# Kernel tuning notes

Measured on AMD Instinct MI355X. Metric: run time of the kernel, lower is better.

Reference implementation:

```python
import jax, jax.numpy as jnp
import numpy as np

N_ATOMS = 20000
N_EDGES = 640000
F = 128          # natom_basis
N_RADIAL = 20
CUTOFF = 5.0


def setup_inputs() -> dict:
    key = jax.random.key(0)
    ks = jax.random.split(key, 10)
    inp = {
        "q": jax.random.normal(ks[0], (N_ATOMS, F), dtype=jnp.float32),
        "mu": jax.random.normal(ks[1], (N_ATOMS, 3, F), dtype=jnp.float32),
        "edge_index": jax.random.randint(ks[2], (2, N_EDGES), 0, N_ATOMS, dtype=jnp.int32),
        "edge_weight": jax.random.normal(ks[3], (N_EDGES, 3), dtype=jnp.float32),
        # interaction_context_network: Linear(F,F) -> SiLU -> Linear(F,3F)
        "W1": jax.random.normal(ks[4], (F, F), dtype=jnp.float32) / np.sqrt(F),
        "b1": jnp.zeros((F,), dtype=jnp.float32),
        "W2": jax.random.normal(ks[5], (F, 3 * F), dtype=jnp.float32) / np.sqrt(F),
        "b2": jnp.zeros((3 * F,), dtype=jnp.float32),
        # filter_network: Linear(n_radial, 3F)
        "Wf": jax.random.normal(ks[6], (N_RADIAL, 3 * F), dtype=jnp.float32) / np.sqrt(N_RADIAL),
        "bf": jnp.zeros((3 * F,), dtype=jnp.float32),
    }
    return inp


def _sinc_radial(d):
    # Bessel/sinc basis: sin(n*pi*d/cutoff)/d, n = 1..n_radial
    n = jnp.arange(1, N_RADIAL + 1, dtype=jnp.float32)  # [R]
    return jnp.sin(d[:, None] * (n * np.pi / CUTOFF)) / d[:, None]  # [E,R]


def _cosine_envelope(d):
    env = 0.5 * (jnp.cos(d * (np.pi / CUTOFF)) + 1.0)
    return jnp.where(d < CUTOFF, env, 0.0)


def reference(q, mu, edge_index, edge_weight, W1, b1, W2, b2, Wf, bf):
    F_ = q.shape[-1]
    # dense per-node context MLP: [N, 3F]
    h = jax.nn.silu(q @ W1 + b1)
    x = h @ W2 + b2

    d = jnp.linalg.norm(edge_weight, axis=-1)              # [E]
    directions = edge_weight / d[:, None]                  # [E,3]
    basis = _sinc_radial(d)                                # [E,R]
    env = _cutoff = _cosine_envelope(d)[:, None]           # [E,1]
    filter_Wij = (basis @ Wf + bf) * env                   # [E,3F]

    idx_i = edge_index[0]
    idx_j = edge_index[1]
    xj = x[idx_j]                                          # [E,3F]
    muj = mu[idx_j]                                        # [E,3,F]

    xe = filter_Wij * xj
    dq, dmuR, dmumu = jnp.split(xe, 3, axis=-1)            # each [E,F]

    q_update = jax.ops.segment_sum(dq, idx_i, num_segments=q.shape[0])

    dmu = dmuR[:, None, :] * directions[:, :, None] + dmumu[:, None, :] * muj  # [E,3,F]
    mu_update = jax.ops.segment_sum(dmu, idx_i, num_segments=mu.shape[0])

    return (q + q_update, mu + mu_update)
```

## Files before the change

### kernel.cpp

```cpp
#include <hip/hip_runtime.h>
#include <hip/hip_bf16.h>

typedef unsigned int uint;
typedef unsigned short ushort;
typedef float v2f __attribute__((ext_vector_type(2)));

#define NATOMS 20000
#define NEDGES 640000
#define FD 128
#define F3 384
#define NR 20
#define MAPB 16
#define GAPB 2

__device__ __forceinline__ uint f2bfu(float f) {
  const uint u = __float_as_uint(f);
  return (u + 0x7FFFu + ((u >> 16) & 1u)) >> 16;
}
__device__ __forceinline__ float bflo(uint u) { return __uint_as_float(u << 16); }
__device__ __forceinline__ float bfhi(uint u) { return __uint_as_float(u & 0xFFFF0000u); }

__global__ __launch_bounds__(256) void hist_kernel(const int* __restrict__ eidx,
                                                   int* __restrict__ cnt) {
  const int e = blockIdx.x * 256 + threadIdx.x;
  if (e < NEDGES) atomicAdd(&cnt[eidx[e]], 1);
}

__global__ __launch_bounds__(512) void scan_kernel(const int* __restrict__ cnt,
                                                   int* __restrict__ off,
                                                   int* __restrict__ cursor) {
  __shared__ int part[512];
  const int t = threadIdx.x;
  const int CH = (NATOMS + 511) / 512;
  const int base = t * CH;
  int s = 0;
  for (int k = 0; k < CH; ++k) {
    const int idx = base + k;
    if (idx < NATOMS) s += cnt[idx];
  }
  part[t] = s;
  __syncthreads();
  if (t == 0) {
    int run = 0;
    for (int i = 0; i < 512; ++i) { const int tmp = part[i]; part[i] = run; run += tmp; }
    off[NATOMS] = run;
  }
  __syncthreads();
  int run = part[t];
  for (int k = 0; k < CH; ++k) {
    const int idx = base + k;
    if (idx < NATOMS) { off[idx] = run; cursor[idx] = run; run += cnt[idx]; }
  }
}

__global__ __launch_bounds__(256) void prep_kernel(
    const int* __restrict__ eidx, const float* __restrict__ ew,
    int* __restrict__ cursor, uint4* __restrict__ basisS)
{
  const int e = blockIdx.x * 256 + threadIdx.x;
  if (e >= NEDGES) return;
  const int i = eidx[e];
  const int j = eidx[NEDGES + e];
  const int pos = atomicAdd(&cursor[i], 1);

  const float w0 = ew[(size_t)e * 3 + 0];
  const float w1 = ew[(size_t)e * 3 + 1];
  const float w2 = ew[(size_t)e * 3 + 2];
  const float d = sqrtf(w0 * w0 + w1 * w1 + w2 * w2);
  const float invd = 1.f / d;
  float s1, c1;
  __sincosf(d * 0.628318530717958f, &s1, &c1);
  const float env = (d < 5.f) ? 0.5f * (c1 + 1.f) : 0.f;

  uint4 r0, r1;
  r0.x = __float_as_uint(s1 * env * invd);
  r0.y = __float_as_uint(2.f * c1);
  r0.z = __float_as_uint(env);
  r0.w = __float_as_uint(w0 * invd);
  r1.x = __float_as_uint(w1 * invd);
  r1.y = __float_as_uint(w2 * invd);
  r1.z = (uint)j;
  r1.w = 0u;
  basisS[(size_t)pos * 2 + 0] = r0;
  basisS[(size_t)pos * 2 + 1] = r1;
}

__global__ __launch_bounds__(128) void mlp_kernel(
    const float* __restrict__ q, const float* __restrict__ mu,
    const float* __restrict__ W1, const float* __restrict__ b1,
    const float* __restrict__ W2, const float* __restrict__ b2v,
    uint* __restrict__ xmp)
{
  __shared__ float qL[MAPB][FD];
  __shared__ float hL[MAPB][FD];
  const int t = threadIdx.x;
  const int a0 = blockIdx.x * MAPB;

  #pragma unroll
  for (int a = 0; a < MAPB; ++a) qL[a][t] = q[(size_t)(a0 + a) * FD + t];
  __syncthreads();

  float hacc[MAPB];
  const float bb1 = b1[t];
  #pragma unroll
  for (int a = 0; a < MAPB; ++a) hacc[a] = bb1;
  for (int i = 0; i < FD; ++i) {
    const float w = W1[(size_t)i * FD + t];
    #pragma unroll
    for (int a = 0; a < MAPB; ++a) hacc[a] += qL[a][i] * w;
  }
  #pragma unroll
  for (int a = 0; a < MAPB; ++a) hL[a][t] = hacc[a] / (1.f + __expf(-hacc[a]));
  __syncthreads();

  float x0[MAPB], x1[MAPB], x2[MAPB];
  const float c0 = b2v[t], c1 = b2v[FD + t], c2 = b2v[2 * FD + t];
  #pragma unroll
  for (int a = 0; a < MAPB; ++a) { x0[a] = c0; x1[a] = c1; x2[a] = c2; }
  for (int i = 0; i < FD; ++i) {
    const float w0 = W2[(size_t)i * F3 + t];
    const float w1 = W2[(size_t)i * F3 + FD + t];
    const float w2 = W2[(size_t)i * F3 + 2 * FD + t];
    #pragma unroll
    for (int a = 0; a < MAPB; ++a) {
      const float hv = hL[a][i];
      x0[a] += hv * w0; x1[a] += hv * w1; x2[a] += hv * w2;
    }
  }
  #pragma unroll
  for (int a = 0; a < MAPB; ++a) {
    const int n = a0 + a;
    const float* ma = mu + (size_t)n * F3;
    const float m0 = ma[t], m1 = ma[FD + t], m2 = ma[2 * FD + t];
    uint* dst = xmp + ((size_t)n * FD + t) * 3;
    dst[0] = f2bfu(x0[a]) | (f2bfu(x1[a]) << 16);
    dst[1] = f2bfu(x2[a]) | (f2bfu(m0) << 16);
    dst[2] = f2bfu(m1)    | (f2bfu(m2) << 16);
  }
}

__global__ __launch_bounds__(128, 3) void gather_kernel(
    const float* __restrict__ q, const float* __restrict__ mu,
    const uint* __restrict__ xmp,
    const float* __restrict__ Wf, const float* __restrict__ bfv,
    const int* __restrict__ off, const uint* __restrict__ basisS,
    float* __restrict__ out)
{
  __shared__ uint stage[64 * 8];
  __shared__ float fb[64][28];
  const int t = threadIdx.x;
  const int a0 = blockIdx.x * GAPB;

  v2f wf0[10], wf1[10], wf2[10];
  #pragma unroll
  for (int r = 0; r < 10; ++r) {
    wf0[r] = (v2f){Wf[(size_t)(2 * r) * F3 + t],       Wf[(size_t)(2 * r + 1) * F3 + t]};
    wf1[r] = (v2f){Wf[(size_t)(2 * r) * F3 + 128 + t], Wf[(size_t)(2 * r + 1) * F3 + 128 + t]};
    wf2[r] = (v2f){Wf[(size_t)(2 * r) * F3 + 256 + t], Wf[(size_t)(2 * r + 1) * F3 + 256 + t]};
  }
  const float bias0 = bfv[t], bias1 = bfv[128 + t], bias2 = bfv[256 + t];

  int a = a0;
  const int beg  = off[a0];
  const int pEnd = off[a0 + GAPB];
  int nxt = off[a + 1];
  float acq = 0.f, ac0 = 0.f, ac1 = 0.f, ac2 = 0.f;
  const size_t NQ = (size_t)NATOMS * FD;

  for (int cb = beg; cb < pEnd; cb += 64) {
    const int nn = min(64, pEnd - cb);
    __syncthreads();
    if (t < nn * 2) ((uint4*)stage)[t] = ((const uint4*)basisS)[(size_t)cb * 2 + t];
    __syncthreads();
    if (t < nn) {
      const uint4 r0 = ((const uint4*)stage)[t * 2];
      const uint4 r1 = ((const uint4*)stage)[t * 2 + 1];
      fb[t][20] = __uint_as_float(r0.z);
      fb[t][21] = __uint_as_float(r0.w);
      fb[t][22] = __uint_as_float(r1.x);
      fb[t][23] = __uint_as_float(r1.y);
      fb[t][24] = __uint_as_float(r1.z);
      float vp = 0.f, vc = __uint_as_float(r0.x);
      const float tc = __uint_as_float(r0.y);
      #pragma unroll
      for (int r = 0; r < NR; ++r) { fb[t][r] = vc; const float vn = tc * vc - vp; vp = vc; vc = vn; }
    }
    __syncthreads();

    uint pX, pY, pZ;
    {
      const uint j0 = __float_as_uint(fb[0][24]);
      const uint* xp = xmp + ((size_t)j0 * FD + t) * 3;
      pX = xp[0]; pY = xp[1]; pZ = xp[2];
    }

    for (int k = 0; k < nn; ++k) {
      const int g = cb + k;
      while (g == nxt) {
        out[(size_t)a * FD + t] = q[(size_t)a * FD + t] + acq;
        const size_t mi = (size_t)a * F3;
        out[NQ + mi + t]       = mu[mi + t]       + ac0;
        out[NQ + mi + 128 + t] = mu[mi + 128 + t] + ac1;
        out[NQ + mi + 256 + t] = mu[mi + 256 + t] + ac2;
        acq = ac0 = ac1 = ac2 = 0.f;
        ++a;
        nxt = (a < NATOMS) ? off[a + 1] : 0x7fffffff;
      }

      uint nX = 0u, nY = 0u, nZ = 0u;
      if (k + 1 < nn) {
        const uint jj = __float_as_uint(fb[k + 1][24]);
        const uint* xp = xmp + ((size_t)jj * FD + t) * 3;
        nX = xp[0]; nY = xp[1]; nZ = xp[2];
      }

      const float* fk = fb[k];
      const float4 M = *(const float4*)(fk + 20);
      v2f s0 = (v2f){0.f, 0.f}, s1 = (v2f){0.f, 0.f}, s2 = (v2f){0.f, 0.f};
      #pragma unroll
      for (int r4 = 0; r4 < 5; ++r4) {
        const float4 bv = ((const float4*)fk)[r4];
        const v2f blo = (v2f){bv.x, bv.y};
        const v2f bhi = (v2f){bv.z, bv.w};
        s0 += blo * wf0[2 * r4]; s0 += bhi * wf0[2 * r4 + 1];
        s1 += blo * wf1[2 * r4]; s1 += bhi * wf1[2 * r4 + 1];
        s2 += blo * wf2[2 * r4]; s2 += bhi * wf2[2 * r4 + 1];
      }
      const float env = M.x;
      const float f0 = s0.x + s0.y + env * bias0;
      const float f1 = s1.x + s1.y + env * bias1;
      const float f2 = s2.x + s2.y + env * bias2;

      acq += f0 * bflo(pX);
      const float dmuR = f1 * bfhi(pX);
      const float dmm  = f2 * bflo(pY);
      ac0 += dmuR * M.y + dmm * bfhi(pY);
      ac1 += dmuR * M.z + dmm * bflo(pZ);
      ac2 += dmuR * M.w + dmm * bfhi(pZ);

      pX = nX; pY = nY; pZ = nZ;
    }
  }
  while (a < a0 + GAPB) {
    out[(size_t)a * FD + t] = q[(size_t)a * FD + t] + acq;
    const size_t mi = (size_t)a * F3;
    out[NQ + mi + t]       = mu[mi + t]       + ac0;
    out[NQ + mi + 128 + t] = mu[mi + 128 + t] + ac1;
    out[NQ + mi + 256 + t] = mu[mi + 256 + t] + ac2;
    acq = ac0 = ac1 = ac2 = 0.f;
    ++a;
  }
}

extern "C" void kernel_launch(void* const* d_in, const int* in_sizes, int n_in,
                              void* d_out, int out_size, void* d_ws, size_t ws_size,
                              hipStream_t stream) {
  const float* q   = (const float*)d_in[0];
  const float* mu  = (const float*)d_in[1];
  const int*   eix = (const int*)d_in[2];
  const float* ew  = (const float*)d_in[3];
  const float* W1  = (const float*)d_in[4];
  const float* b1  = (const float*)d_in[5];
  const float* W2  = (const float*)d_in[6];
  const float* b2v = (const float*)d_in[7];
  const float* Wf  = (const float*)d_in[8];
  const float* bfv = (const float*)d_in[9];
  float* out = (float*)d_out;

  char* w = (char*)d_ws;
  uint* basisS = (uint*)w;  w += (size_t)NEDGES * 32;
  uint* xmp    = (uint*)w;  w += (size_t)NATOMS * FD * 3 * sizeof(uint);
  int*  off    = (int*)w;   w += (size_t)(NATOMS + 1) * sizeof(int);
  int*  cnt    = (int*)w;   w += (size_t)NATOMS * sizeof(int);
  int*  cursor = (int*)w;

  hipMemsetAsync(cnt, 0, (size_t)NATOMS * sizeof(int), stream);

  hist_kernel<<<(NEDGES + 255) / 256, 256, 0, stream>>>(eix, cnt);
  scan_kernel<<<1, 512, 0, stream>>>(cnt, off, cursor);
  prep_kernel<<<(NEDGES + 255) / 256, 256, 0, stream>>>(eix, ew, cursor,
                                                        (uint4*)basisS);

  mlp_kernel<<<NATOMS / MAPB, 128, 0, stream>>>(q, mu, W1, b1, W2, b2v, xmp);

  gather_kernel<<<NATOMS / GAPB, 128, 0, stream>>>(q, mu, xmp, Wf, bfv,
                                                   off, basisS, out);
}
```

Before: 480.7 us.

## Merge edge prep and node MLP into one launch with vectorized LDS reads

```diff
diff --git a/kernel.cpp b/kernel.cpp
--- a/kernel.cpp
+++ b/kernel.cpp
@@ -10,8 +10,9 @@
 #define FD 128
 #define F3 384
 #define NR 20
-#define MAPB 16
 #define GAPB 2
+#define PREP_BLOCKS ((NEDGES + 255) / 256)
+#define MLP_BLOCKS  (NATOMS / 32)
 
 __device__ __forceinline__ uint f2bfu(float f) {
   const uint u = __float_as_uint(f);
@@ -53,86 +54,107 @@
   }
 }
 
-__global__ __launch_bounds__(256) void prep_kernel(
+__global__ __launch_bounds__(256, 4) void prep_mlp_kernel(
     const int* __restrict__ eidx, const float* __restrict__ ew,
-    int* __restrict__ cursor, uint4* __restrict__ basisS)
-{
-  const int e = blockIdx.x * 256 + threadIdx.x;
-  if (e >= NEDGES) return;
-  const int i = eidx[e];
-  const int j = eidx[NEDGES + e];
-  const int pos = atomicAdd(&cursor[i], 1);
-
-  const float w0 = ew[(size_t)e * 3 + 0];
-  const float w1 = ew[(size_t)e * 3 + 1];
-  const float w2 = ew[(size_t)e * 3 + 2];
-  const float d = sqrtf(w0 * w0 + w1 * w1 + w2 * w2);
-  const float invd = 1.f / d;
-  float s1, c1;
-  __sincosf(d * 0.628318530717958f, &s1, &c1);
-  const float env = (d < 5.f) ? 0.5f * (c1 + 1.f) : 0.f;
-
-  uint4 r0, r1;
-  r0.x = __float_as_uint(s1 * env * invd);
-  r0.y = __float_as_uint(2.f * c1);
-  r0.z = __float_as_uint(env);
-  r0.w = __float_as_uint(w0 * invd);
-  r1.x = __float_as_uint(w1 * invd);
-  r1.y = __float_as_uint(w2 * invd);
-  r1.z = (uint)j;
-  r1.w = 0u;
-  basisS[(size_t)pos * 2 + 0] = r0;
-  basisS[(size_t)pos * 2 + 1] = r1;
-}
-
-__global__ __launch_bounds__(128) void mlp_kernel(
+    int* __restrict__ cursor, uint4* __restrict__ basisS,
     const float* __restrict__ q, const float* __restrict__ mu,
     const float* __restrict__ W1, const float* __restrict__ b1,
     const float* __restrict__ W2, const float* __restrict__ b2v,
     uint* __restrict__ xmp)
 {
-  __shared__ float qL[MAPB][FD];
-  __shared__ float hL[MAPB][FD];
+  __shared__ float qL[2][16][FD];
+  __shared__ float hL[2][16][FD];
+
   const int t = threadIdx.x;
-  const int a0 = blockIdx.x * MAPB;
-
-  #pragma unroll
-  for (int a = 0; a < MAPB; ++a) qL[a][t] = q[(size_t)(a0 + a) * FD + t];
+
+  if (blockIdx.x < PREP_BLOCKS) {
+    const int e = blockIdx.x * 256 + t;
+    if (e >= NEDGES) return;
+    const int i = eidx[e];
+    const int j = eidx[NEDGES + e];
+    const int pos = atomicAdd(&cursor[i], 1);
+
+    const float w0 = ew[(size_t)e * 3 + 0];
+    const float w1 = ew[(size_t)e * 3 + 1];
+    const float w2 = ew[(size_t)e * 3 + 2];
+    const float d = sqrtf(w0 * w0 + w1 * w1 + w2 * w2);
+    const float invd = 1.f / d;
+    float s1, c1;
+    __sincosf(d * 0.628318530717958f, &s1, &c1);
+    const float env = (d < 5.f) ? 0.5f * (c1 + 1.f) : 0.f;
+
+    uint4 r0, r1;
+    r0.x = __float_as_uint(s1 * env * invd);
+    r0.y = __float_as_uint(2.f * c1);
+    r0.z = __float_as_uint(env);
+    r0.w = __float_as_uint(w0 * invd);
+    r1.x = __float_as_uint(w1 * invd);
+    r1.y = __float_as_uint(w2 * invd);
+    r1.z = (uint)j;
+    r1.w = 0u;
+    basisS[(size_t)pos * 2 + 0] = r0;
+    basisS[(size_t)pos * 2 + 1] = r1;
+    return;
+  }
+
+  const int half = t >> 7;
+  const int tc = t & 127;
+  const int a0 = (blockIdx.x - PREP_BLOCKS) * 32 + half * 16;
+
+  #pragma unroll
+  for (int a = 0; a < 16; ++a) qL[half][a][tc] = q[(size_t)(a0 + a) * FD + tc];
   __syncthreads();
 
-  float hacc[MAPB];
-  const float bb1 = b1[t];
-  #pragma unroll
-  for (int a = 0; a < MAPB; ++a) hacc[a] = bb1;
-  for (int i = 0; i < FD; ++i) {
-    const float w = W1[(size_t)i * FD + t];
+  float hacc[16];
+  const float bb1 = b1[tc];
+  #pragma unroll
+  for (int a = 0; a < 16; ++a) hacc[a] = bb1;
+  for (int i = 0; i < FD; i += 4) {
+    const float w0 = W1[(size_t)i * FD + tc];
+    const float w1 = W1[(size_t)(i + 1) * FD + tc];
+    const float w2 = W1[(size_t)(i + 2) * FD + tc];
+    const float w3 = W1[(size_t)(i + 3) * FD + tc];
     #pragma unroll
-    for (int a = 0; a < MAPB; ++a) hacc[a] += qL[a][i] * w;
-  }
-  #pragma unroll
-  for (int a = 0; a < MAPB; ++a) hL[a][t] = hacc[a] / (1.f + __expf(-hacc[a]));
+    for (int a = 0; a < 16; ++a) {
+      const float4 qv = *(const float4*)&qL[half][a][i];
+      hacc[a] += qv.x * w0 + qv.y * w1 + qv.z * w2 + qv.w * w3;
+    }
+  }
+  #pragma unroll
+  for (int a = 0; a < 16; ++a) hL[half][a][tc] = hacc[a] / (1.f + __expf(-hacc[a]));
   __syncthreads();
 
-  float x0[MAPB], x1[MAPB], x2[MAPB];
-  const float c0 = b2v[t], c1 = b2v[FD + t], c2 = b2v[2 * FD + t];
-  #pragma unroll
-  for (int a = 0; a < MAPB; ++a) { x0[a] = c0; x1[a] = c1; x2[a] = c2; }
-  for (int i = 0; i < FD; ++i) {
-    const float w0 = W2[(size_t)i * F3 + t];
-    const float w1 = W2[(size_t)i * F3 + FD + t];
-    const float w2 = W2[(size_t)i * F3 + 2 * FD + t];
+  float x0[16], x1[16], x2[16];
+  const float c0 = b2v[tc], c1 = b2v[FD + tc], c2 = b2v[2 * FD + tc];
+  #pragma unroll
+  for (int a = 0; a < 16; ++a) { x0[a] = c0; x1[a] = c1; x2[a] = c2; }
+  for (int i = 0; i < FD; i += 4) {
+    const float wa0 = W2[(size_t)i * F3 + tc];
+    const float wa1 = W2[(size_t)(i + 1) * F3 + tc];
+    const float wa2 = W2[(size_t)(i + 2) * F3 + tc];
+    const float wa3 = W2[(size_t)(i + 3) * F3 + tc];
+    const float wb0 = W2[(size_t)i * F3 + FD + tc];
+    const float wb1 = W2[(size_t)(i + 1) * F3 + FD + tc];
+    const float wb2 = W2[(size_t)(i + 2) * F3 + FD + tc];
+    const float wb3 = W2[(size_t)(i + 3) * F3 + FD + tc];
+    const float wc0 = W2[(size_t)i * F3 + 2 * FD + tc];
+    const float wc1 = W2[(size_t)(i + 1) * F3 + 2 * FD + tc];
+    const float wc2 = W2[(size_t)(i + 2) * F3 + 2 * FD + tc];
+    const float wc3 = W2[(size_t)(i + 3) * F3 + 2 * FD + tc];
     #pragma unroll
-    for (int a = 0; a < MAPB; ++a) {
-      const float hv = hL[a][i];
-      x0[a] += hv * w0; x1[a] += hv * w1; x2[a] += hv * w2;
-    }
-  }
-  #pragma unroll
-  for (int a = 0; a < MAPB; ++a) {
+    for (int a = 0; a < 16; ++a) {
+      const float4 hv = *(const float4*)&hL[half][a][i];
+      x0[a] += hv.x * wa0 + hv.y * wa1 + hv.z * wa2 + hv.w * wa3;
+      x1[a] += hv.x * wb0 + hv.y * wb1 + hv.z * wb2 + hv.w * wb3;
+      x2[a] += hv.x * wc0 + hv.y * wc1 + hv.z * wc2 + hv.w * wc3;
+    }
+  }
+  #pragma unroll
+  for (int a = 0; a < 16; ++a) {
     const int n = a0 + a;
     const float* ma = mu + (size_t)n * F3;
-    const float m0 = ma[t], m1 = ma[FD + t], m2 = ma[2 * FD + t];
-    uint* dst = xmp + ((size_t)n * FD + t) * 3;
+    const float m0 = ma[tc], m1 = ma[FD + tc], m2 = ma[2 * FD + tc];
+    uint* dst = xmp + ((size_t)n * FD + tc) * 3;
     dst[0] = f2bfu(x0[a]) | (f2bfu(x1[a]) << 16);
     dst[1] = f2bfu(x2[a]) | (f2bfu(m0) << 16);
     dst[2] = f2bfu(m1)    | (f2bfu(m2) << 16);
@@ -278,10 +300,9 @@
 
   hist_kernel<<<(NEDGES + 255) / 256, 256, 0, stream>>>(eix, cnt);
   scan_kernel<<<1, 512, 0, stream>>>(cnt, off, cursor);
-  prep_kernel<<<(NEDGES + 255) / 256, 256, 0, stream>>>(eix, ew, cursor,
-                                                        (uint4*)basisS);
-
-  mlp_kernel<<<NATOMS / MAPB, 128, 0, stream>>>(q, mu, W1, b1, W2, b2v, xmp);
+
+  prep_mlp_kernel<<<PREP_BLOCKS + MLP_BLOCKS, 256, 0, stream>>>(
+      eix, ew, cursor, (uint4*)basisS, q, mu, W1, b1, W2, b2v, xmp);
 
   gather_kernel<<<NATOMS / GAPB, 128, 0, stream>>>(q, mu, xmp, Wf, bfv,
                                                    off, basisS, out);
```

Measured after the change: 506.1 us. 5.3% more time.

## Move edge basis math into gather, unroll MLP loads, double-buffer gather prefetch

Applied to the files above, without the earlier changes.

```diff
diff --git a/kernel.cpp b/kernel.cpp
--- a/kernel.cpp
+++ b/kernel.cpp
@@ -63,26 +63,12 @@
   const int j = eidx[NEDGES + e];
   const int pos = atomicAdd(&cursor[i], 1);
 
-  const float w0 = ew[(size_t)e * 3 + 0];
-  const float w1 = ew[(size_t)e * 3 + 1];
-  const float w2 = ew[(size_t)e * 3 + 2];
-  const float d = sqrtf(w0 * w0 + w1 * w1 + w2 * w2);
-  const float invd = 1.f / d;
-  float s1, c1;
-  __sincosf(d * 0.628318530717958f, &s1, &c1);
-  const float env = (d < 5.f) ? 0.5f * (c1 + 1.f) : 0.f;
-
-  uint4 r0, r1;
-  r0.x = __float_as_uint(s1 * env * invd);
-  r0.y = __float_as_uint(2.f * c1);
-  r0.z = __float_as_uint(env);
-  r0.w = __float_as_uint(w0 * invd);
-  r1.x = __float_as_uint(w1 * invd);
-  r1.y = __float_as_uint(w2 * invd);
-  r1.z = (uint)j;
-  r1.w = 0u;
-  basisS[(size_t)pos * 2 + 0] = r0;
-  basisS[(size_t)pos * 2 + 1] = r1;
+  uint4 r;
+  r.x = __float_as_uint(ew[(size_t)e * 3 + 0]);
+  r.y = __float_as_uint(ew[(size_t)e * 3 + 1]);
+  r.z = __float_as_uint(ew[(size_t)e * 3 + 2]);
+  r.w = (uint)j;
+  basisS[pos] = r;
 }
 
 __global__ __launch_bounds__(128) void mlp_kernel(
@@ -104,10 +90,16 @@
   const float bb1 = b1[t];
   #pragma unroll
   for (int a = 0; a < MAPB; ++a) hacc[a] = bb1;
-  for (int i = 0; i < FD; ++i) {
-    const float w = W1[(size_t)i * FD + t];
+  for (int i = 0; i < FD; i += 4) {
+    const float w0 = W1[(size_t)i * FD + t];
+    const float w1 = W1[(size_t)(i + 1) * FD + t];
+    const float w2 = W1[(size_t)(i + 2) * FD + t];
+    const float w3 = W1[(size_t)(i + 3) * FD + t];
     #pragma unroll
-    for (int a = 0; a < MAPB; ++a) hacc[a] += qL[a][i] * w;
+    for (int a = 0; a < MAPB; ++a) {
+      const float4 qv = *(const float4*)&qL[a][i];
+      hacc[a] += qv.x * w0 + qv.y * w1 + qv.z * w2 + qv.w * w3;
+    }
   }
   #pragma unroll
   for (int a = 0; a < MAPB; ++a) hL[a][t] = hacc[a] / (1.f + __expf(-hacc[a]));
@@ -117,14 +109,25 @@
   const float c0 = b2v[t], c1 = b2v[FD + t], c2 = b2v[2 * FD + t];
   #pragma unroll
   for (int a = 0; a < MAPB; ++a) { x0[a] = c0; x1[a] = c1; x2[a] = c2; }
-  for (int i = 0; i < FD; ++i) {
-    const float w0 = W2[(size_t)i * F3 + t];
-    const float w1 = W2[(size_t)i * F3 + FD + t];
-    const float w2 = W2[(size_t)i * F3 + 2 * FD + t];
+  for (int i = 0; i < FD; i += 4) {
+    const float wa0 = W2[(size_t)i * F3 + t];
+    const float wa1 = W2[(size_t)(i + 1) * F3 + t];
+    const float wa2 = W2[(size_t)(i + 2) * F3 + t];
+    const float wa3 = W2[(size_t)(i + 3) * F3 + t];
+    const float wb0 = W2[(size_t)i * F3 + FD + t];
+    const float wb1 = W2[(size_t)(i + 1) * F3 + FD + t];
+    const float wb2 = W2[(size_t)(i + 2) * F3 + FD + t];
+    const float wb3 = W2[(size_t)(i + 3) * F3 + FD + t];
+    const float wc0 = W2[(size_t)i * F3 + 2 * FD + t];
+    const float wc1 = W2[(size_t)(i + 1) * F3 + 2 * FD + t];
+    const float wc2 = W2[(size_t)(i + 2) * F3 + 2 * FD + t];
+    const float wc3 = W2[(size_t)(i + 3) * F3 + 2 * FD + t];
     #pragma unroll
     for (int a = 0; a < MAPB; ++a) {
-      const float hv = hL[a][i];
-      x0[a] += hv * w0; x1[a] += hv * w1; x2[a] += hv * w2;
+      const float4 hv = *(const float4*)&hL[a][i];
+      x0[a] += hv.x * wa0 + hv.y * wa1 + hv.z * wa2 + hv.w * wa3;
+      x1[a] += hv.x * wb0 + hv.y * wb1 + hv.z * wb2 + hv.w * wb3;
+      x2[a] += hv.x * wc0 + hv.y * wc1 + hv.z * wc2 + hv.w * wc3;
     }
   }
   #pragma unroll
@@ -143,10 +146,10 @@
     const float* __restrict__ q, const float* __restrict__ mu,
     const uint* __restrict__ xmp,
     const float* __restrict__ Wf, const float* __restrict__ bfv,
-    const int* __restrict__ off, const uint* __restrict__ basisS,
+    const int* __restrict__ off, const uint4* __restrict__ basisS,
     float* __restrict__ out)
 {
-  __shared__ uint stage[64 * 8];
+  __shared__ uint4 stage[64];
   __shared__ float fb[64][28];
   const int t = threadIdx.x;
   const int a0 = blockIdx.x * GAPB;
@@ -167,78 +170,105 @@
   float acq = 0.f, ac0 = 0.f, ac1 = 0.f, ac2 = 0.f;
   const size_t NQ = (size_t)NATOMS * FD;
 
+  auto edge_compute = [&](int k, uint pX, uint pY, uint pZ) {
+    const float* fk = fb[k];
+    const float4 M = *(const float4*)(fk + 20);
+    v2f s0 = (v2f){0.f, 0.f}, s1 = (v2f){0.f, 0.f}, s2 = (v2f){0.f, 0.f};
+    #pragma unroll
+    for (int r4 = 0; r4 < 5; ++r4) {
+      const float4 bv = ((const float4*)fk)[r4];
+      const v2f blo = (v2f){bv.x, bv.y};
+      const v2f bhi = (v2f){bv.z, bv.w};
+      s0 += blo * wf0[2 * r4]; s0 += bhi * wf0[2 * r4 + 1];
+      s1 += blo * wf1[2 * r4]; s1 += bhi * wf1[2 * r4 + 1];
+      s2 += blo * wf2[2 * r4]; s2 += bhi * wf2[2 * r4 + 1];
+    }
+    const float env = M.x;
+    const float f0 = s0.x + s0.y + env * bias0;
+    const float f1 = s1.x + s1.y + env * bias1;
+    const float f2 = s2.x + s2.y + env * bias2;
+
+    acq += f0 * bflo(pX);
+    const float dmuR = f1 * bfhi(pX);
+    const float dmm  = f2 * bflo(pY);
+    ac0 += dmuR * M.y + dmm * bfhi(pY);
+    ac1 += dmuR * M.z + dmm * bflo(pZ);
+    ac2 += dmuR * M.w + dmm * bfhi(pZ);
+  };
+
+  auto flush_to = [&](int g) {
+    while (g == nxt) {
+      out[(size_t)a * FD + t] = q[(size_t)a * FD + t] + acq;
+      const size_t mi = (size_t)a * F3;
+      out[NQ + mi + t]       = mu[mi + t]       + ac0;
+      out[NQ + mi + 128 + t] = mu[mi + 128 + t] + ac1;
+      out[NQ + mi + 256 + t] = mu[mi + 256 + t] + ac2;
+      acq = ac0 = ac1 = ac2 = 0.f;
+      ++a;
+      nxt = (a < NATOMS) ? off[a + 1] : 0x7fffffff;
+    }
+  };
+
   for (int cb = beg; cb < pEnd; cb += 64) {
     const int nn = min(64, pEnd - cb);
     __syncthreads();
-    if (t < nn * 2) ((uint4*)stage)[t] = ((const uint4*)basisS)[(size_t)cb * 2 + t];
+    if (t < nn) stage[t] = basisS[cb + t];
     __syncthreads();
     if (t < nn) {
-      const uint4 r0 = ((const uint4*)stage)[t * 2];
-      const uint4 r1 = ((const uint4*)stage)[t * 2 + 1];
-      fb[t][20] = __uint_as_float(r0.z);
-      fb[t][21] = __uint_as_float(r0.w);
-      fb[t][22] = __uint_as_float(r1.x);
-      fb[t][23] = __uint_as_float(r1.y);
-      fb[t][24] = __uint_as_float(r1.z);
-      float vp = 0.f, vc = __uint_as_float(r0.x);
-      const float tc = __uint_as_float(r0.y);
+      const uint4 r = stage[t];
+      const float w0 = __uint_as_float(r.x);
+      const float w1 = __uint_as_float(r.y);
+      const float w2 = __uint_as_float(r.z);
+      const float d = sqrtf(w0 * w0 + w1 * w1 + w2 * w2);
+      const float invd = 1.f / d;
+      float s1v, c1v;
+      __sincosf(d * 0.628318530717958f, &s1v, &c1v);
+      const float env = (d < 5.f) ? 0.5f * (c1v + 1.f) : 0.f;
+      fb[t][20] = env;
+      fb[t][21] = w0 * invd;
+      fb[t][22] = w1 * invd;
+      fb[t][23] = w2 * invd;
+      fb[t][24] = __uint_as_float(r.w);
+      float vp = 0.f, vc = s1v * env * invd;
+      const float tc2 = 2.f * c1v;
       #pragma unroll
-      for (int r = 0; r < NR; ++r) { fb[t][r] = vc; const float vn = tc * vc - vp; vp = vc; vc = vn; }
+      for (int r2 = 0; r2 < NR; ++r2) { fb[t][r2] = vc; const float vn = tc2 * vc - vp; vp = vc; vc = vn; }
     }
     __syncthreads();
 
-    uint pX, pY, pZ;
+    uint aX, aY, aZ, bX, bY, bZ;
     {
       const uint j0 = __float_as_uint(fb[0][24]);
       const uint* xp = xmp + ((size_t)j0 * FD + t) * 3;
-      pX = xp[0]; pY = xp[1]; pZ = xp[2];
-    }
-
-    for (int k = 0; k < nn; ++k) {
-      const int g = cb + k;
-      while (g == nxt) {
-        out[(size_t)a * FD + t] = q[(size_t)a * FD + t] + acq;
-        const size_t mi = (size_t)a * F3;
-        out[NQ + mi + t]       = mu[mi + t]       + ac0;
-        out[NQ + mi + 128 + t] = mu[mi + 128 + t] + ac1;
-        out[NQ + mi + 256 + t] = mu[mi + 256 + t] + ac2;
-        acq = ac0 = ac1 = ac2 = 0.f;
-        ++a;
-        nxt = (a < NATOMS) ? off[a + 1] : 0x7fffffff;
+      aX = xp[0]; aY = xp[1]; aZ = xp[2];
+      const int k1 = (nn > 1) ? 1 : 0;
+      const uint j1 = __float_as_uint(fb[k1][24]);
+      const uint* yp = xmp + ((size_t)j1 * FD + t) * 3;
+      bX = yp[0]; bY = yp[1]; bZ = yp[2];
+    }
+
+    int k = 0;
+    while (k < nn) {
+      {
+        flush_to(cb + k);
+        const uint cX = aX, cY = aY, cZ = aZ;
+        const int kp = (k + 2 < nn) ? k + 2 : nn - 1;
+        const uint jj = __float_as_uint(fb[kp][24]);
+        const uint* xp = xmp + ((size_t)jj * FD + t) * 3;
+        aX = xp[0]; aY = xp[1]; aZ = xp[2];
+        edge_compute(k, cX, cY, cZ);
       }
-
-      uint nX = 0u, nY = 0u, nZ = 0u;
-      if (k + 1 < nn) {
-        const uint jj = __float_as_uint(fb[k + 1][24]);
+      if (++k >= nn) break;
+      {
+        flush_to(cb + k);
+        const uint cX = bX, cY = bY, cZ = bZ;
+        const int kp = (k + 2 < nn) ? k + 2 : nn - 1;
+        const uint jj = __float_as_uint(fb[kp][24]);
         const uint* xp = xmp + ((size_t)jj * FD + t) * 3;
-        nX = xp[0]; nY = xp[1]; nZ = xp[2];
+        bX = xp[0]; bY = xp[1]; bZ = xp[2];
+        edge_compute(k, cX, cY, cZ);
       }
-
-      const float* fk = fb[k];
-      const float4 M = *(const float4*)(fk + 20);
-      v2f s0 = (v2f){0.f, 0.f}, s1 = (v2f){0.f, 0.f}, s2 = (v2f){0.f, 0.f};
-      #pragma unroll
-      for (int r4 = 0; r4 < 5; ++r4) {
-        const float4 bv = ((const float4*)fk)[r4];
-        const v2f blo = (v2f){bv.x, bv.y};
-        const v2f bhi = (v2f){bv.z, bv.w};
-        s0 += blo * wf0[2 * r4]; s0 += bhi * wf0[2 * r4 + 1];
-        s1 += blo * wf1[2 * r4]; s1 += bhi * wf1[2 * r4 + 1];
-        s2 += blo * wf2[2 * r4]; s2 += bhi * wf2[2 * r4 + 1];
-      }
-      const float env = M.x;
-      const float f0 = s0.x + s0.y + env * bias0;
-      const float f1 = s1.x + s1.y + env * bias1;
-      const float f2 = s2.x + s2.y + env * bias2;
-
-      acq += f0 * bflo(pX);
-      const float dmuR = f1 * bfhi(pX);
-      const float dmm  = f2 * bflo(pY);
-      ac0 += dmuR * M.y + dmm * bfhi(pY);
-      ac1 += dmuR * M.z + dmm * bflo(pZ);
-      ac2 += dmuR * M.w + dmm * bfhi(pZ);
-
-      pX = nX; pY = nY; pZ = nZ;
+      ++k;
     }
   }
   while (a < a0 + GAPB) {
@@ -268,18 +298,17 @@
   float* out = (float*)d_out;
 
   char* w = (char*)d_ws;
-  uint* basisS = (uint*)w;  w += (size_t)NEDGES * 32;
-  uint* xmp    = (uint*)w;  w += (size_t)NATOMS * FD * 3 * sizeof(uint);
-  int*  off    = (int*)w;   w += (size_t)(NATOMS + 1) * sizeof(int);
-  int*  cnt    = (int*)w;   w += (size_t)NATOMS * sizeof(int);
-  int*  cursor = (int*)w;
+  uint4* basisS = (uint4*)w; w += (size_t)NEDGES * 16;
+  uint*  xmp    = (uint*)w;  w += (size_t)NATOMS * FD * 3 * sizeof(uint);
+  int*   off    = (int*)w;   w += (size_t)(NATOMS + 1) * sizeof(int);
+  int*   cnt    = (int*)w;   w += (size_t)NATOMS * sizeof(int);
+  int*   cursor = (int*)w;
 
   hipMemsetAsync(cnt, 0, (size_t)NATOMS * sizeof(int), stream);
 
   hist_kernel<<<(NEDGES + 255) / 256, 256, 0, stream>>>(eix, cnt);
   scan_kernel<<<1, 512, 0, stream>>>(cnt, off, cursor);
-  prep_kernel<<<(NEDGES + 255) / 256, 256, 0, stream>>>(eix, ew, cursor,
-                                                        (uint4*)basisS);
+  prep_kernel<<<(NEDGES + 255) / 256, 256, 0, stream>>>(eix, ew, cursor, basisS);
 
   mlp_kernel<<<NATOMS / MAPB, 128, 0, stream>>>(q, mu, W1, b1, W2, b2v, xmp);
 
```

Result: no change. 486.5 us (+1.2%).
